# Performance work log

Hardware: AMD Instinct MI355X
Metric: run time of the kernel (lower is better)

## Reference

```python
import jax, jax.numpy as jnp
import numpy as np

D_MODEL = 512
DQ = D_MODEL // 4  # 128
TIME_SHIFT_START = 256
VELOCITY_START = 768
NOTE_OFF_START = 128


def conv1d(x, w, b, stride, pad):
    # x: [B, Cin, L], w: [Cout, Cin, K]
    y = jax.lax.conv_general_dilated(x, w, (stride,), [(pad, pad)],
                                     dimension_numbers=('NCH', 'OIH', 'NCH'))
    return y + b[None, :, None]


def adaptive_avg_pool1d(x, out_size):
    # faithful to torch AdaptiveAvgPool1d bin boundaries
    L = x.shape[-1]
    starts = (np.arange(out_size) * L) // out_size
    ends = np.ceil((np.arange(out_size) + 1) * L / out_size).astype(np.int64)
    cs = jnp.concatenate([jnp.zeros(x.shape[:-1] + (1,), x.dtype),
                          jnp.cumsum(x, axis=-1)], axis=-1)
    return (cs[..., ends] - cs[..., starts]) / jnp.asarray(ends - starts, x.dtype)


def setup_inputs() -> dict:
    key = jax.random.key(0)
    ks = jax.random.split(key, 20)

    def w(k, shape):
        fan_in = int(np.prod(shape[1:]))
        return jax.random.normal(k, shape, jnp.float32) / np.sqrt(fan_in)

    def b(k, n):
        return jax.random.normal(k, (n,), jnp.float32) * 0.01

    return {
        'tokens': jax.random.randint(ks[0], (32, 4096), 0, 774),
        'r1_w': w(ks[1], (32, 1, 8)),    'r1_b': b(ks[2], 32),
        'r2_w': w(ks[3], (64, 32, 4)),   'r2_b': b(ks[4], 64),
        'h1_w': w(ks[5], (64, 128, 12)), 'h1_b': b(ks[6], 64),
        'h2_w': w(ks[7], (32, 64, 8)),   'h2_b': b(ks[8], 32),
        'm1_w': w(ks[9], (64, 128, 5)),  'm1_b': b(ks[10], 64),
        'm2_w': w(ks[11], (32, 64, 3)),  'm2_b': b(ks[12], 32),
        'd1_w': w(ks[13], (16, 6, 4)),   'd1_b': b(ks[14], 16),
        'd2_w': w(ks[15], (16, 16, 3)),  'd2_b': b(ks[16], 16),
        'fc_w': w(ks[17], (D_MODEL, D_MODEL)), 'fc_b': b(ks[18], D_MODEL),
    }


def reference(tokens, r1_w, r1_b, r2_w, r2_b, h1_w, h1_b, h2_w, h2_b,
              m1_w, m1_b, m2_w, m2_b, d1_w, d1_b, d2_w, d2_b, fc_w, fc_b):
    B, S = tokens.shape
    relu = jax.nn.relu

    # rhythm: binary time-shift indicator [B,1,S]
    ts = ((tokens >= TIME_SHIFT_START) & (tokens < VELOCITY_START)).astype(jnp.float32)[:, None, :]
    r = relu(conv1d(ts, r1_w, r1_b, 2, 3))
    r = relu(conv1d(r, r2_w, r2_b, 2, 1))
    r = adaptive_avg_pool1d(r, DQ).reshape(B, -1)  # [B, 64*DQ]

    # vectorized one-hot pitch scatter (replaces the python double loop): [B,128,S]
    nm = tokens < NOTE_OFF_START
    pitch = jnp.transpose(
        jax.nn.one_hot(jnp.where(nm, tokens, 0) % 128, 128, dtype=jnp.float32)
        * nm[..., None].astype(jnp.float32), (0, 2, 1))

    h = relu(conv1d(pitch, h1_w, h1_b, 1, 6))
    h = relu(conv1d(h, h2_w, h2_b, 2, 3))
    h = adaptive_avg_pool1d(h, DQ).reshape(B, -1)  # [B, 32*DQ]

    m = relu(conv1d(pitch, m1_w, m1_b, 1, 2))
    m = relu(conv1d(m, m2_w, m2_b, 1, 1))
    m = adaptive_avg_pool1d(m, DQ).reshape(B, -1)  # [B, 32*DQ]

    # velocity one-hot scatter: [B,6,S]
    vm = tokens >= VELOCITY_START
    vel = jnp.clip(jnp.where(vm, tokens - VELOCITY_START, 0), 0, 5)
    vpat = jnp.transpose(
        jax.nn.one_hot(vel, 6, dtype=jnp.float32) * vm[..., None].astype(jnp.float32),
        (0, 2, 1))
    d = relu(conv1d(vpat, d1_w, d1_b, 1, 2))
    d = relu(conv1d(d, d2_w, d2_b, 1, 1))
    d = adaptive_avg_pool1d(d, DQ).reshape(B, -1)  # [B, 16*DQ]

    # total flattened size is 36*d_model != d_model, so torch branch always pools
    r, h, m, d = [adaptive_avg_pool1d(f[:, None, :], DQ)[:, 0] for f in (r, h, m, d)]

    combined = jnp.concatenate([r, h, m, d], axis=1)       # [B, d_model]
    feats = combined @ fc_w.T + fc_b                        # Linear
    return jnp.broadcast_to(feats[:, None, :], (B, S, D_MODEL))
```

## Files before the change

kernel.cpp:

```cpp
#include <hip/hip_runtime.h>

typedef unsigned short u16;
typedef unsigned int u32;
typedef float vf4 __attribute__((ext_vector_type(4)));
typedef unsigned int vu4 __attribute__((ext_vector_type(4)));
typedef short sh8 __attribute__((ext_vector_type(8)));
typedef float f32x4 __attribute__((ext_vector_type(4)));

__device__ __forceinline__ float bf2f(u16 u) {
  return __uint_as_float(((u32)u) << 16);
}
__device__ __forceinline__ u16 f2bf(float f) {
  u32 x = __float_as_uint(f);
  return (u16)((x + 0x7fffu + ((x >> 16) & 1u)) >> 16);
}
__device__ __forceinline__ float ldin(const void* p, int idx, int isf) {
  return isf ? ((const float*)p)[idx] : bf2f(((const u16*)p)[idx]);
}

#define OFF_FLAG  ((size_t)0)
#define OFF_WB    ((size_t)16)
#define OFF_WTH1  ((size_t)1180432)
#define OFF_WTM1  ((size_t)1576720)
#define OFF_COMB  ((size_t)1741840)
#define OFF_FEATF ((size_t)1807376)
#define OFF_FEATB ((size_t)1872912)
#define OFF_DP    ((size_t)18686736)
#define OFF_WH2B  ((size_t)52536080)
#define OFF_WH2L  ((size_t)52568848)
#define OFF_WM2B  ((size_t)52601616)
#define OFF_WM2L  ((size_t)52613904)
#define WS_NEEDED ((size_t)52626192)

#define WB_R1W 0
#define WB_R1B 256
#define WB_R2W 288
#define WB_R2B 8480
#define WB_H1B 8544
#define WB_H2W 8608
#define WB_H2B 24992
#define WB_M1B 25024
#define WB_M2W 25088
#define WB_M2B 31232
#define WB_D1W 31264
#define WB_D1B 31648
#define WB_D2W 31664
#define WB_D2B 32432
#define WB_FCW 32448
#define WB_FCB 294592
#define WB_TOTAL 295104

#define CV_TH1_END 394176
#define CV_TM1_END 435456
#define CV_CMB_END 451840
#define CV_WH2_END 468224
#define CV_TOTAL   474368

__global__ __launch_bounds__(256) void k_convert(
    const void* r1_w, const void* r1_b, const void* r2_w, const void* r2_b,
    const void* h1_w, const void* h1_b, const void* h2_w, const void* h2_b,
    const void* m1_w, const void* m1_b, const void* m2_w, const void* m2_b,
    const void* d1_w, const void* d1_b, const void* d2_w, const void* d2_b,
    const void* fc_w, const void* fc_b,
    int* __restrict__ flagp, float* __restrict__ wb,
    float* __restrict__ wTh1, float* __restrict__ wTm1,
    float* __restrict__ combined,
    u16* __restrict__ wh2b, u16* __restrict__ wh2l,
    u16* __restrict__ wm2b, u16* __restrict__ wm2l) {
  __shared__ int cnt[4];
  int tid = threadIdx.x;
  {
    u16 v = ((const u16*)fc_w)[2 * tid];
    int e = (v >> 7) & 0xFF;
    int outside = (e < 100 || e > 140) ? 1 : 0;
    unsigned long long m = __ballot(outside);
    if ((tid & 63) == 0) cnt[tid >> 6] = __popcll(m);
  }
  __syncthreads();
  int isf = (cnt[0] + cnt[1] + cnt[2] + cnt[3] >= 64) ? 1 : 0;
  if (blockIdx.x == 0 && tid == 0) flagp[0] = isf;

  int j = blockIdx.x * 256 + tid;
  if (j >= CV_TOTAL) return;
  if (j < WB_TOTAL) {
    const void* src; int si;
    if      (j < WB_R1B) { src = r1_w; si = j; }
    else if (j < WB_R2W) { src = r1_b; si = j - WB_R1B; }
    else if (j < WB_R2B) { src = r2_w; si = j - WB_R2W; }
    else if (j < WB_H1B) { src = r2_b; si = j - WB_R2B; }
    else if (j < WB_H2W) { src = h1_b; si = j - WB_H1B; }
    else if (j < WB_H2B) { src = h2_w; si = j - WB_H2W; }
    else if (j < WB_M1B) { src = h2_b; si = j - WB_H2B; }
    else if (j < WB_M2W) { src = m1_b; si = j - WB_M1B; }
    else if (j < WB_M2B) { src = m2_w; si = j - WB_M2W; }
    else if (j < WB_D1W) { src = m2_b; si = j - WB_M2B; }
    else if (j < WB_D1B) { src = d1_w; si = j - WB_D1W; }
    else if (j < WB_D2W) { src = d1_b; si = j - WB_D1B; }
    else if (j < WB_D2B) { src = d2_w; si = j - WB_D2W; }
    else if (j < WB_FCW) { src = d2_b; si = j - WB_D2B; }
    else if (j < WB_FCB) { src = fc_w; si = j - WB_FCW; }
    else                 { src = fc_b; si = j - WB_FCB; }
    wb[j] = ldin(src, si, isf);
  } else if (j < CV_TH1_END) {
    int j2 = j - WB_TOTAL;
    int o = j2 & 63, r = j2 >> 6;
    wTh1[j2] = (r >= 1536) ? 0.f : ldin(h1_w, (o * 128 + r / 12) * 12 + (r % 12), isf);
  } else if (j < CV_TM1_END) {
    int j3 = j - CV_TH1_END;
    int o = j3 & 63, r = j3 >> 6;
    wTm1[j3] = (r >= 640) ? 0.f : ldin(m1_w, (o * 128 + r / 5) * 5 + (r % 5), isf);
  } else if (j < CV_CMB_END) {
    combined[j - CV_TM1_END] = 0.f;
  } else if (j < CV_WH2_END) {
    int jj = j - CV_CMB_END;
    int o = jj >> 9, rem = jj & 511, c = rem >> 3, kk = rem & 7;
    float w = ldin(h2_w, (o * 64 + c) * 8 + kk, isf);
    u16 hi = f2bf(w);
    wh2b[jj] = hi;
    wh2l[jj] = f2bf(w - bf2f(hi));
  } else {
    int jj = j - CV_WH2_END;
    int o = jj / 192, rem = jj % 192, c = rem / 3, kk = rem % 3;
    float w = ldin(m2_w, (o * 64 + c) * 3 + kk, isf);
    u16 hi = f2bf(w);
    wm2b[jj] = hi;
    wm2l[jj] = f2bf(w - bf2f(hi));
  }
}


#define HT_STRIDE 142
#define MT_STRIDE 133

__device__ __forceinline__ void dev_hf(float* smem, const int* tok,
                                       const float* wTh1, const float* h1bf,
                                       const u16* wh2b, const u16* wh2l,
                                       const float* h2bf,
                                       float* combined, int chunk, int q, int b) {
  u16* htile = (u16*)smem;
  int* tks = (int*)(smem + 4544);
  const int tid = threadIdx.x;
  const int tb = q * 512 + chunk * 64;
  const int sg0 = 2 * tb;
  const int* tokb = tok + b * 4096;
  if (tid < 146) {
    int x = sg0 - 9 + tid;
    int p = ((unsigned)x < 4096u) ? tokb[x] : 128;
    tks[tid] = (p < 128 ? p : 128) * 768;
  }
  __syncthreads();
  {
    const int og = tid & 15, slot = tid >> 4;
    const float4 bias = *(const float4*)(h1bf + og * 4);
    const float* wbase = wTh1 + og * 4;
    for (int pos = slot; pos < 134; pos += 16) {
      int t = sg0 - 3 + pos;
      u16 o0 = 0, o1 = 0, o2 = 0, o3 = 0;
      if ((unsigned)t <= 4096u) {
        float4 acc = bias;
#pragma unroll
        for (int k = 0; k < 12; ++k) {
          const float4 wv = *(const float4*)(wbase + tks[pos + k] + k * 64);
          acc.x += wv.x; acc.y += wv.y; acc.z += wv.z; acc.w += wv.w;
        }
        o0 = f2bf(fmaxf(acc.x, 0.f)); o1 = f2bf(fmaxf(acc.y, 0.f));
        o2 = f2bf(fmaxf(acc.z, 0.f)); o3 = f2bf(fmaxf(acc.w, 0.f));
      }
      int rb = og * 4 * HT_STRIDE + pos;
      htile[rb] = o0;
      htile[rb + HT_STRIDE] = o1;
      htile[rb + 2 * HT_STRIDE] = o2;
      htile[rb + 3 * HT_STRIDE] = o3;
    }
  }
  __syncthreads();
  const int w = tid >> 6, l = tid & 63;
  const int quad = l >> 4, n = l & 15;
  const int ot = w & 1, tp = w >> 1;
  f32x4 acc2[2];
  acc2[0] = (f32x4){0.f, 0.f, 0.f, 0.f};
  acc2[1] = (f32x4){0.f, 0.f, 0.f, 0.f};
  const u16* wph = wh2b + (size_t)(16 * ot + n) * 512 + quad * 8;
  const u16* wpl = wh2l + (size_t)(16 * ot + n) * 512 + quad * 8;
  const u32* hp = (const u32*)htile;
  for (int kc = 0; kc < 2; ++kc) {
    sh8 ah[8], al[8];
#pragma unroll
    for (int s = 0; s < 8; ++s) {
      ah[s] = *(const sh8*)(wph + kc * 256 + 32 * s);
      al[s] = *(const sh8*)(wpl + kc * 256 + 32 * s);
    }
#pragma unroll
    for (int it = 0; it < 2; ++it) {
      int fb = 16 * (2 * it + tp) + n;
#pragma unroll
      for (int s = 0; s < 8; ++s) {
        int c = kc * 32 + 4 * s + quad;
        const u32* p = hp + c * 71 + fb;
        u32 bw[4] = {p[0], p[1], p[2], p[3]};
        sh8 bb;
        __builtin_memcpy(&bb, bw, 16);
        acc2[it] = __builtin_amdgcn_mfma_f32_16x16x32_bf16(ah[s], bb, acc2[it], 0, 0, 0);
        acc2[it] = __builtin_amdgcn_mfma_f32_16x16x32_bf16(al[s], bb, acc2[it], 0, 0, 0);
      }
    }
  }
#pragma unroll
  for (int r = 0; r < 4; ++r) {
    float bsv = h2bf[16 * ot + quad * 4 + r];
    float s = fmaxf(acc2[0][r] + bsv, 0.f) + fmaxf(acc2[1][r] + bsv, 0.f);
    s += __shfl_xor(s, 1, 64);
    s += __shfl_xor(s, 2, 64);
    s += __shfl_xor(s, 4, 64);
    s += __shfl_xor(s, 8, 64);
    if (n == 0) {
      int o = 16 * ot + quad * 4 + r;
      atomicAdd(&combined[b * 512 + 128 + 4 * o + q], s * (1.f / 512.f));
    }
  }
}

__device__ __forceinline__ void dev_mf(float* smem, const int* tok,
                                       const float* wTm1, const float* m1bf,
                                       const u16* wm2b, const u16* wm2l,
                                       const float* m2bf,
                                       float* combined, int sub, int q, int b) {
  u16* mtile = (u16*)smem;
  int* tks = (int*)(smem + 4256);
  const int tid = threadIdx.x;
  const int tb = q * 1024 + sub * 128;
  const int* tokb = tok + b * 4096;
  if (tid < 135) {
    int x = tb - 4 + tid;
    int p = ((unsigned)x < 4096u) ? tokb[x] : 128;
    tks[tid] = (p < 128 ? p : 128) * 320;
  }
  __syncthreads();
  {
    const int og = tid & 15, slot = tid >> 4;
    const float4 bias = *(const float4*)(m1bf + og * 4);
    const float* wbase = wTm1 + og * 4;
    for (int u = slot; u < 131; u += 16) {
      int t = tb - 2 + u;
      u16 o0 = 0, o1 = 0, o2 = 0, o3 = 0;
      if ((unsigned)t < 4096u) {
        float4 acc = bias;
#pragma unroll
        for (int k = 0; k < 5; ++k) {
          const float4 wv = *(const float4*)(wbase + tks[u + k] + k * 64);
          acc.x += wv.x; acc.y += wv.y; acc.z += wv.z; acc.w += wv.w;
        }
        o0 = f2bf(fmaxf(acc.x, 0.f)); o1 = f2bf(fmaxf(acc.y, 0.f));
        o2 = f2bf(fmaxf(acc.z, 0.f)); o3 = f2bf(fmaxf(acc.w, 0.f));
      }
      int rb = og * 4 * MT_STRIDE + u;
      mtile[rb] = o0;
      mtile[rb + MT_STRIDE] = o1;
      mtile[rb + 2 * MT_STRIDE] = o2;
      mtile[rb + 3 * MT_STRIDE] = o3;
    }
  }
  __syncthreads();
  const int w = tid >> 6, l = tid & 63;
  const int quad = l >> 4, n = l & 15;
  const int ot = w & 1, tp = w >> 1;
  sh8 ah[6], al[6];
  {
    const u16* wph = wm2b + (size_t)(16 * ot + n) * 192 + quad * 8;
    const u16* wpl = wm2l + (size_t)(16 * ot + n) * 192 + quad * 8;
#pragma unroll
    for (int s = 0; s < 6; ++s) {
      ah[s] = *(const sh8*)(wph + 32 * s);
      al[s] = *(const sh8*)(wpl + 32 * s);
    }
  }
  float bsv[4];
#pragma unroll
  for (int r = 0; r < 4; ++r) bsv[r] = m2bf[16 * ot + quad * 4 + r];
  float sm[4] = {0.f, 0.f, 0.f, 0.f};
  const int gkb = quad * 8;
  for (int it = 0; it < 4; ++it) {
    int ub = 16 * (2 * it + tp) + n + 1;
    f32x4 acc = {0.f, 0.f, 0.f, 0.f};
#pragma unroll
    for (int s = 0; s < 6; ++s) {
      sh8 bb;
#pragma unroll
      for (int j = 0; j < 8; ++j) {
        int gk = 32 * s + gkb + j;
        int c = (gk * 21846) >> 16;
        int kk = gk - 3 * c;
        bb[j] = (short)mtile[c * MT_STRIDE + ub + kk];
      }
      acc = __builtin_amdgcn_mfma_f32_16x16x32_bf16(ah[s], bb, acc, 0, 0, 0);
      acc = __builtin_amdgcn_mfma_f32_16x16x32_bf16(al[s], bb, acc, 0, 0, 0);
    }
#pragma unroll
    for (int r = 0; r < 4; ++r) sm[r] += fmaxf(acc[r] + bsv[r], 0.f);
  }
#pragma unroll
  for (int r = 0; r < 4; ++r) {
    float s = sm[r];
    s += __shfl_xor(s, 1, 64);
    s += __shfl_xor(s, 2, 64);
    s += __shfl_xor(s, 4, 64);
    s += __shfl_xor(s, 8, 64);
    if (n == 0) {
      int o = 16 * ot + quad * 4 + r;
      atomicAdd(&combined[b * 512 + 256 + 4 * o + q], s * (1.f / 1024.f));
    }
  }
}

__device__ __forceinline__ void dev_rf(float* smem, const int* tok,
                                       const float* r1wf, const float* r1bf,
                                       const float* r2wf, const float* r2bf,
                                       float* combined, int chunk, int b) {
  float* w1s = smem;
  float* b1s = smem + 256;
  float* Ibuf = smem + 288;
  float* r1t = smem + 560;
  float* wcr = smem + 4848;
  const int tid = threadIdx.x;
  const int tbase = chunk * 64;
  const int tk0 = 4 * tbase - 7;
  const int* tokb = tok + b * 4096;
  w1s[tid] = r1wf[tid];
  if (tid < 32) b1s[tid] = r1bf[tid];
  for (int i = tid; i < 270; i += 256) {
    int x = tk0 + i;
    float v = 0.f;
    if ((unsigned)x < 4096u) {
      int tk = tokb[x];
      v = (tk >= 256 && tk < 768) ? 1.f : 0.f;
    }
    Ibuf[i] = v;
  }
  __syncthreads();
  {
    const int tl1 = tid & 63, og1 = tid >> 6;
    for (int xi = tl1; xi < 134; xi += 64) {
      int x = 2 * tbase - 2 + xi;
      if ((unsigned)x < 2048u) {
        float iv[8];
#pragma unroll
        for (int k = 0; k < 8; ++k) iv[k] = Ibuf[2 * xi + k];
#pragma unroll
        for (int i = 0; i < 8; ++i) {
          int o = og1 * 8 + i;
          float a = b1s[o];
#pragma unroll
          for (int k = 0; k < 8; ++k) a = fmaf(w1s[o * 8 + k], iv[k], a);
          r1t[o * 134 + xi] = fmaxf(a, 0.f);
        }
      } else {
#pragma unroll
        for (int i = 0; i < 8; ++i) r1t[(og1 * 8 + i) * 134 + xi] = 0.f;
      }
    }
  }
  __syncthreads();
  const int half = chunk >> 3;
  const int og = tid >> 6, tl = tid & 63;
  float acc[16];
#pragma unroll
  for (int i = 0; i < 16; ++i) acc[i] = 0.f;
  for (int c0 = 0; c0 < 32; c0 += 8) {
    for (int f = tid; f < 2048; f += 256) {
      int o = f & 63, r = f >> 6, k = r & 3, cc = r >> 2;
      wcr[f] = r2wf[(o * 32 + c0 + cc) * 4 + k];
    }
    __syncthreads();
#pragma unroll
    for (int cc = 0; cc < 8; ++cc) {
      const float* rr = r1t + (c0 + cc) * 134 + 2 * tl;
      float ev[3], od[3];
#pragma unroll
      for (int f3 = 0; f3 < 3; ++f3) {
        ev[f3] = rr[2 * f3];
        od[f3] = rr[2 * f3 + 1];
      }
#pragma unroll
      for (int k = 0; k < 4; ++k) {
        const int p = (k + 1) & 1, fk = (k + 1) >> 1;
        const float* wv = &wcr[(cc * 4 + k) * 64 + og * 16];
        float4 wa = *(const float4*)wv;
        float4 wbv = *(const float4*)(wv + 4);
        float4 wcc = *(const float4*)(wv + 8);
        float4 wd4 = *(const float4*)(wv + 12);
        float wr[16] = {wa.x, wa.y, wa.z, wa.w, wbv.x, wbv.y, wbv.z, wbv.w,
                        wcc.x, wcc.y, wcc.z, wcc.w, wd4.x, wd4.y, wd4.z, wd4.w};
        float v0 = p ? od[fk] : ev[fk];
#pragma unroll
        for (int i = 0; i < 16; ++i) acc[i] = fmaf(v0, wr[i], acc[i]);
      }
    }
    __syncthreads();
  }
  const float inv = 1.f / 512.f;
#pragma unroll
  for (int i = 0; i < 16; ++i) {
    int o = og * 16 + i;
    float s = fmaxf(acc[i] + r2bf[o], 0.f);
#pragma unroll
    for (int d = 32; d > 0; d >>= 1) s += __shfl_down(s, d, 64);
    if (tl == 0) atomicAdd(&combined[b * 512 + 2 * o + half], s * inv);
  }
}

__device__ __forceinline__ void dev_df(float* smem, const int* tok,
                                       const float* d1wf, const float* d1bf,
                                       const float* d2wf, const float* d2bf,
                                       float* dpws, int chunk, int b) {
  float* wds7 = smem;
  float* wd = smem + 448;
  int* cls = (int*)(smem + 1216);
  float (*dt)[132] = reinterpret_cast<float(*)[132]>(smem + 1352);
  float* c2 = smem + 3464;
  const int tid = threadIdx.x;
  const int tbase = chunk * 128;
  const int* tokb = tok + b * 4096;
  for (int f = tid; f < 448; f += 256) {
    int k = f & 3, rest = f >> 2, v = rest % 7, c = rest / 7;
    wds7[f] = (v < 6) ? d1wf[(c * 6 + v) * 4 + k] : 0.f;
  }
  for (int f = tid; f < 768; f += 256) wd[f] = d2wf[f];
  if (tid < 136) {
    int x = tbase - 3 + tid;
    int v = 6;
    if ((unsigned)x < 4096u) {
      int tk = tokb[x];
      if (tk >= 768) { v = tk - 768; v = v > 5 ? 5 : v; } else v = 6;
    }
    cls[tid] = v;
  }
  __syncthreads();
  for (int f = tid; f < 16 * 131; f += 256) {
    int iu = f % 131, c = f / 131;
    int x = tbase - 1 + iu;
    float v = 0.f;
    if (x >= 0 && x <= 4096) {
      float a = d1bf[c];
#pragma unroll
      for (int k = 0; k < 4; ++k) {
        a += wds7[(c * 7 + cls[iu + k]) * 4 + k];
      }
      v = fmaxf(a, 0.f);
    }
    dt[c][iu] = v;
  }
  __syncthreads();
  for (int idx = tid; idx < 16 * 129; idx += 256) {
    int o = idx / 129, tl = idx % 129;
    float a = d2bf[o];
    const float* ww = &wd[o * 48];
#pragma unroll 4
    for (int c = 0; c < 16; ++c) {
      a = fmaf(dt[c][tl], ww[c * 3 + 0],
          fmaf(dt[c][tl + 1], ww[c * 3 + 1],
          fmaf(dt[c][tl + 2], ww[c * 3 + 2], a)));
    }
    c2[o * 133 + tl] = fmaxf(a, 0.f);
  }
  __syncthreads();
  if (tid < 64) {
    int o = tid >> 2, qq = tid & 3;
    const float* row = c2 + o * 133 + 32 * qq;
    float s = 0.f;
#pragma unroll
    for (int j = 0; j < 33; ++j) s += row[j];
    dpws[(size_t)(b * 16 + o) * 128 + 4 * chunk + qq] = s * (1.f / 33.f);
  }
}

__global__ __launch_bounds__(256, 4) void k_fused(const int* __restrict__ tok,
                                                  const float* __restrict__ wb,
                                                  const float* __restrict__ wTh1,
                                                  const float* __restrict__ wTm1,
                                                  const u16* __restrict__ wh2b,
                                                  const u16* __restrict__ wh2l,
                                                  const u16* __restrict__ wm2b,
                                                  const u16* __restrict__ wm2l,
                                                  float* __restrict__ combined,
                                                  float* __restrict__ dpws) {
  __shared__ __align__(16) float smem[6896];
  int bx = blockIdx.x;
  if (bx < 1024) {
    dev_hf(smem, tok, wTh1, wb + WB_H1B, wh2b, wh2l, wb + WB_H2B, combined,
           bx & 7, (bx >> 3) & 3, bx >> 5);
  } else if (bx < 2048) {
    int n = bx - 1024;
    dev_mf(smem, tok, wTm1, wb + WB_M1B, wm2b, wm2l, wb + WB_M2B, combined,
           n & 7, (n >> 3) & 3, n >> 5);
  } else if (bx < 2560) {
    int n = bx - 2048;
    dev_rf(smem, tok, wb + WB_R1W, wb + WB_R1B, wb + WB_R2W, wb + WB_R2B,
           combined, n & 15, n >> 4);
  } else {
    int n = bx - 2560;
    dev_df(smem, tok, wb + WB_D1W, wb + WB_D1B, wb + WB_D2W, wb + WB_D2B,
           dpws, n & 31, n >> 5);
  }
}

__global__ __launch_bounds__(256) void k_fc(const float* __restrict__ combined,
                                            const float* __restrict__ dpws,
                                            const float* __restrict__ fcwf,
                                            const float* __restrict__ fcbf,
                                            float* __restrict__ featf,
                                            u16* __restrict__ featb) {
  const int bx = blockIdx.x;
  const int b = bx >> 3, oct = bx & 7;
  const int tid = threadIdx.x;
  __shared__ float cb[512];
  cb[tid] = combined[b * 512 + tid];
  if (tid < 128) {
    cb[256 + tid] = combined[b * 512 + 256 + tid];
  } else {
    int j = tid - 128;
    int o = j >> 3, i0 = (j & 7) * 16;
    const float* row = dpws + (size_t)(b * 16 + o) * 128;
    float s = 0.f;
#pragma unroll
    for (int i = 0; i < 16; ++i) s += row[i0 + i];
    cb[384 + j] = s * (1.f / 16.f);
  }
  __syncthreads();
  const int oo = oct * 64 + (tid >> 2), part = tid & 3;
  float acc = 0.f;
  const float4* wr = (const float4*)(fcwf + (size_t)oo * 512 + part * 128);
#pragma unroll 8
  for (int j4 = 0; j4 < 32; ++j4) {
    float4 w = wr[j4];
    const float* c4 = &cb[part * 128 + j4 * 4];
    acc = fmaf(c4[0], w.x, acc);
    acc = fmaf(c4[1], w.y, acc);
    acc = fmaf(c4[2], w.z, acc);
    acc = fmaf(c4[3], w.w, acc);
  }
  acc += __shfl_xor(acc, 1, 64);
  acc += __shfl_xor(acc, 2, 64);
  if (part == 0) {
    float r = acc + fcbf[oo];
    featf[b * 512 + oo] = r;
    featb[b * 512 + oo] = f2bf(r);
  }
}

__global__ __launch_bounds__(256) void k_bcast(const int* __restrict__ flagp,
                                               const vf4* __restrict__ featf4,
                                               const vu4* __restrict__ featb4,
                                               vf4* __restrict__ outf,
                                               vu4* __restrict__ outb) {
  if (flagp[0]) {
    int base = blockIdx.x * 1024 + threadIdx.x;
#pragma unroll
    for (int s = 0; s < 4; ++s) {
      int g = base + s * 256;
      vf4 v = featf4[(g >> 19) * 128 + (g & 127)];
      __builtin_nontemporal_store(v, &outf[g]);
    }
  } else {
    int base = blockIdx.x * 512 + threadIdx.x;
#pragma unroll
    for (int s = 0; s < 2; ++s) {
      int g = base + s * 256;
      vu4 v = featb4[(g >> 18) * 64 + (g & 63)];
      __builtin_nontemporal_store(v, &outb[g]);
    }
  }
}

extern "C" void kernel_launch(void* const* d_in, const int* in_sizes, int n_in,
                              void* d_out, int out_size, void* d_ws, size_t ws_size,
                              hipStream_t stream) {
  if (ws_size < WS_NEEDED) return;

  const int* tokens = (const int*)d_in[0];
  const void* r1_w = d_in[1];  const void* r1_b = d_in[2];
  const void* r2_w = d_in[3];  const void* r2_b = d_in[4];
  const void* h1_w = d_in[5];  const void* h1_b = d_in[6];
  const void* h2_w = d_in[7];  const void* h2_b = d_in[8];
  const void* m1_w = d_in[9];  const void* m1_b = d_in[10];
  const void* m2_w = d_in[11]; const void* m2_b = d_in[12];
  const void* d1_w = d_in[13]; const void* d1_b = d_in[14];
  const void* d2_w = d_in[15]; const void* d2_b = d_in[16];
  const void* fc_w = d_in[17]; const void* fc_b = d_in[18];

  char* ws = (char*)d_ws;
  int*   flagp   = (int*)  (ws + OFF_FLAG);
  float* wb      = (float*)(ws + OFF_WB);
  float* wTh1    = (float*)(ws + OFF_WTH1);
  float* wTm1    = (float*)(ws + OFF_WTM1);
  float* combined= (float*)(ws + OFF_COMB);
  float* featf   = (float*)(ws + OFF_FEATF);
  u16*   featb   = (u16*)  (ws + OFF_FEATB);
  float* dpws    = (float*)(ws + OFF_DP);
  u16*   wh2b    = (u16*)  (ws + OFF_WH2B);
  u16*   wh2l    = (u16*)  (ws + OFF_WH2L);
  u16*   wm2b    = (u16*)  (ws + OFF_WM2B);
  u16*   wm2l    = (u16*)  (ws + OFF_WM2L);

  k_convert<<<1853, 256, 0, stream>>>(r1_w, r1_b, r2_w, r2_b, h1_w, h1_b, h2_w, h2_b,
                                      m1_w, m1_b, m2_w, m2_b, d1_w, d1_b, d2_w, d2_b,
                                      fc_w, fc_b, flagp, wb, wTh1, wTm1, combined,
                                      wh2b, wh2l, wm2b, wm2l);
  k_fused<<<3584, 256, 0, stream>>>(tokens, wb, wTh1, wTm1, wh2b, wh2l, wm2b, wm2l,
                                    combined, dpws);
  k_fc<<<256, 256, 0, stream>>>(combined, dpws, wb + WB_FCW, wb + WB_FCB, featf, featb);
  k_bcast<<<16384, 256, 0, stream>>>(flagp, (const vf4*)featf, (const vu4*)featb,
                                     (vf4*)d_out, (vu4*)d_out);
}
```

Baseline: 392.3 us.

## Fuse FC into broadcast kernel and interleave branch blocks in fused conv kernel

Merges the FC and broadcast kernels into one, so each of 2048 blocks recomputes a 64-output slice of the linear layer and writes it straight to 512 sequence rows. This drops one launch and the feature round trip through workspace. The FC work is now repeated 8 times per batch/octet, and the store pattern changes. Separately, the fused conv kernel's block index is interleaved modulo 7, so the heavy and light branches mix across the schedule and load balance better.

```diff
diff --git a/kernel.cpp b/kernel.cpp
--- a/kernel.cpp
+++ b/kernel.cpp
@@ -23,8 +23,6 @@
 #define OFF_WTH1  ((size_t)1180432)
 #define OFF_WTM1  ((size_t)1576720)
 #define OFF_COMB  ((size_t)1741840)
-#define OFF_FEATF ((size_t)1807376)
-#define OFF_FEATB ((size_t)1872912)
 #define OFF_DP    ((size_t)18686736)
 #define OFF_WH2B  ((size_t)52536080)
 #define OFF_WH2L  ((size_t)52568848)
@@ -485,34 +483,38 @@
                                                   float* __restrict__ dpws) {
   __shared__ __align__(16) float smem[6896];
   int bx = blockIdx.x;
-  if (bx < 1024) {
+  int s7 = bx % 7, i7 = bx / 7;
+  if (s7 < 2) {
+    int n = s7 * 512 + i7;
     dev_hf(smem, tok, wTh1, wb + WB_H1B, wh2b, wh2l, wb + WB_H2B, combined,
-           bx & 7, (bx >> 3) & 3, bx >> 5);
-  } else if (bx < 2048) {
-    int n = bx - 1024;
+           n & 7, (n >> 3) & 3, n >> 5);
+  } else if (s7 < 4) {
+    int n = (s7 - 2) * 512 + i7;
     dev_mf(smem, tok, wTm1, wb + WB_M1B, wm2b, wm2l, wb + WB_M2B, combined,
            n & 7, (n >> 3) & 3, n >> 5);
-  } else if (bx < 2560) {
-    int n = bx - 2048;
+  } else if (s7 < 5) {
+    int n = i7;
     dev_rf(smem, tok, wb + WB_R1W, wb + WB_R1B, wb + WB_R2W, wb + WB_R2B,
            combined, n & 15, n >> 4);
   } else {
-    int n = bx - 2560;
+    int n = (s7 - 5) * 512 + i7;
     dev_df(smem, tok, wb + WB_D1W, wb + WB_D1B, wb + WB_D2W, wb + WB_D2B,
            dpws, n & 31, n >> 5);
   }
 }
 
-__global__ __launch_bounds__(256) void k_fc(const float* __restrict__ combined,
-                                            const float* __restrict__ dpws,
-                                            const float* __restrict__ fcwf,
-                                            const float* __restrict__ fcbf,
-                                            float* __restrict__ featf,
-                                            u16* __restrict__ featb) {
+__global__ __launch_bounds__(256) void k_out(const int* __restrict__ flagp,
+                                             const float* __restrict__ combined,
+                                             const float* __restrict__ dpws,
+                                             const float* __restrict__ fcwf,
+                                             const float* __restrict__ fcbf,
+                                             float* __restrict__ outf,
+                                             u16* __restrict__ outb) {
   const int bx = blockIdx.x;
-  const int b = bx >> 3, oct = bx & 7;
+  const int s8 = bx & 7, oct = (bx >> 3) & 7, b = bx >> 6;
   const int tid = threadIdx.x;
   __shared__ float cb[512];
+  __shared__ float feat[64];
   cb[tid] = combined[b * 512 + tid];
   if (tid < 128) {
     cb[256 + tid] = combined[b * 512 + 256 + tid];
@@ -540,33 +542,29 @@
   }
   acc += __shfl_xor(acc, 1, 64);
   acc += __shfl_xor(acc, 2, 64);
-  if (part == 0) {
-    float r = acc + fcbf[oo];
-    featf[b * 512 + oo] = r;
-    featb[b * 512 + oo] = f2bf(r);
-  }
-}
-
-__global__ __launch_bounds__(256) void k_bcast(const int* __restrict__ flagp,
-                                               const vf4* __restrict__ featf4,
-                                               const vu4* __restrict__ featb4,
-                                               vf4* __restrict__ outf,
-                                               vu4* __restrict__ outb) {
+  if (part == 0) feat[tid >> 2] = acc + fcbf[oo];
+  __syncthreads();
+  const size_t obase = ((size_t)b * 4096 + (size_t)s8 * 512) * 512 + oct * 64;
   if (flagp[0]) {
-    int base = blockIdx.x * 1024 + threadIdx.x;
-#pragma unroll
-    for (int s = 0; s < 4; ++s) {
-      int g = base + s * 256;
-      vf4 v = featf4[(g >> 19) * 128 + (g & 127)];
-      __builtin_nontemporal_store(v, &outf[g]);
+    const int slot = tid & 15, rowg = tid >> 4;
+    float4 v4 = *(const float4*)&feat[slot * 4];
+    vf4 vv; vv[0] = v4.x; vv[1] = v4.y; vv[2] = v4.z; vv[3] = v4.w;
+    float* op = outf + obase + (size_t)rowg * 512 + slot * 4;
+#pragma unroll 8
+    for (int it = 0; it < 32; ++it) {
+      __builtin_nontemporal_store(vv, (vf4*)(op + (size_t)it * 16 * 512));
     }
   } else {
-    int base = blockIdx.x * 512 + threadIdx.x;
-#pragma unroll
-    for (int s = 0; s < 2; ++s) {
-      int g = base + s * 256;
-      vu4 v = featb4[(g >> 18) * 64 + (g & 63)];
-      __builtin_nontemporal_store(v, &outb[g]);
+    const int slot = tid & 7, rowg = tid >> 3;
+    u32 w0 = (u32)f2bf(feat[slot * 8 + 0]) | ((u32)f2bf(feat[slot * 8 + 1]) << 16);
+    u32 w1 = (u32)f2bf(feat[slot * 8 + 2]) | ((u32)f2bf(feat[slot * 8 + 3]) << 16);
+    u32 w2 = (u32)f2bf(feat[slot * 8 + 4]) | ((u32)f2bf(feat[slot * 8 + 5]) << 16);
+    u32 w3 = (u32)f2bf(feat[slot * 8 + 6]) | ((u32)f2bf(feat[slot * 8 + 7]) << 16);
+    vu4 vv; vv[0] = w0; vv[1] = w1; vv[2] = w2; vv[3] = w3;
+    u16* op = outb + obase + (size_t)rowg * 512 + slot * 8;
+#pragma unroll 8
+    for (int it = 0; it < 16; ++it) {
+      __builtin_nontemporal_store(vv, (vu4*)(op + (size_t)it * 32 * 512));
     }
   }
 }
@@ -593,8 +591,6 @@
   float* wTh1    = (float*)(ws + OFF_WTH1);
   float* wTm1    = (float*)(ws + OFF_WTM1);
   float* combined= (float*)(ws + OFF_COMB);
-  float* featf   = (float*)(ws + OFF_FEATF);
-  u16*   featb   = (u16*)  (ws + OFF_FEATB);
   float* dpws    = (float*)(ws + OFF_DP);
   u16*   wh2b    = (u16*)  (ws + OFF_WH2B);
   u16*   wh2l    = (u16*)  (ws + OFF_WH2L);
@@ -607,7 +603,6 @@
                                       wh2b, wh2l, wm2b, wm2l);
   k_fused<<<3584, 256, 0, stream>>>(tokens, wb, wTh1, wTm1, wh2b, wh2l, wm2b, wm2l,
                                     combined, dpws);
-  k_fc<<<256, 256, 0, stream>>>(combined, dpws, wb + WB_FCW, wb + WB_FCB, featf, featb);
-  k_bcast<<<16384, 256, 0, stream>>>(flagp, (const vf4*)featf, (const vu4*)featb,
-                                     (vf4*)d_out, (vu4*)d_out);
-}
+  k_out<<<2048, 256, 0, stream>>>(flagp, combined, dpws, wb + WB_FCW, wb + WB_FCB,
+                                  (float*)d_out, (u16*)d_out);
+}
```

After: 403.2 us. 1.03x slower.

## Transpose m-branch tile to time-major layout for vectorized MFMA operand loads

Applied to the files above, without the earlier changes.

Reorders the m2 weight layout to [kk][o][c] and stores the conv1 output tile time-major (time rows, 64 channels, padded stride 72). Each thread can then load an 8-element bf16 MFMA B operand with one vector LDS read instead of eight scalar gathered reads with division arithmetic. Conv1 outputs are written as a packed 64-bit store. This costs a slightly larger shared-memory footprint and changes the tks offset.

```diff
diff --git a/kernel.cpp b/kernel.cpp
--- a/kernel.cpp
+++ b/kernel.cpp
@@ -120,7 +120,7 @@
     wh2l[jj] = f2bf(w - bf2f(hi));
   } else {
     int jj = j - CV_WH2_END;
-    int o = jj / 192, rem = jj % 192, c = rem / 3, kk = rem % 3;
+    int kk = jj >> 11, rem = jj & 2047, o = rem >> 6, c = rem & 63;
     float w = ldin(m2_w, (o * 64 + c) * 3 + kk, isf);
     u16 hi = f2bf(w);
     wm2b[jj] = hi;
@@ -130,7 +130,7 @@
 
 
 #define HT_STRIDE 142
-#define MT_STRIDE 133
+#define MT2_STRIDE 72
 
 __device__ __forceinline__ void dev_hf(float* smem, const int* tok,
                                        const float* wTh1, const float* h1bf,
@@ -225,8 +225,8 @@
                                        const u16* wm2b, const u16* wm2l,
                                        const float* m2bf,
                                        float* combined, int sub, int q, int b) {
-  u16* mtile = (u16*)smem;
-  int* tks = (int*)(smem + 4256);
+  u16* mT = (u16*)smem;
+  int* tks = (int*)(smem + 4716);
   const int tid = threadIdx.x;
   const int tb = q * 1024 + sub * 128;
   const int* tokb = tok + b * 4096;
@@ -253,47 +253,45 @@
         o0 = f2bf(fmaxf(acc.x, 0.f)); o1 = f2bf(fmaxf(acc.y, 0.f));
         o2 = f2bf(fmaxf(acc.z, 0.f)); o3 = f2bf(fmaxf(acc.w, 0.f));
       }
-      int rb = og * 4 * MT_STRIDE + u;
-      mtile[rb] = o0;
-      mtile[rb + MT_STRIDE] = o1;
-      mtile[rb + 2 * MT_STRIDE] = o2;
-      mtile[rb + 3 * MT_STRIDE] = o3;
+      uint2 pack;
+      pack.x = (u32)o0 | ((u32)o1 << 16);
+      pack.y = (u32)o2 | ((u32)o3 << 16);
+      *(uint2*)&mT[u * MT2_STRIDE + og * 4] = pack;
     }
   }
   __syncthreads();
   const int w = tid >> 6, l = tid & 63;
   const int quad = l >> 4, n = l & 15;
   const int ot = w & 1, tp = w >> 1;
-  sh8 ah[6], al[6];
+  sh8 ah[3][2], al[3][2];
   {
-    const u16* wph = wm2b + (size_t)(16 * ot + n) * 192 + quad * 8;
-    const u16* wpl = wm2l + (size_t)(16 * ot + n) * 192 + quad * 8;
-#pragma unroll
-    for (int s = 0; s < 6; ++s) {
-      ah[s] = *(const sh8*)(wph + 32 * s);
-      al[s] = *(const sh8*)(wpl + 32 * s);
+    const u16* wph = wm2b + (size_t)(16 * ot + n) * 64 + quad * 8;
+    const u16* wpl = wm2l + (size_t)(16 * ot + n) * 64 + quad * 8;
+#pragma unroll
+    for (int kk = 0; kk < 3; ++kk) {
+#pragma unroll
+      for (int kc = 0; kc < 2; ++kc) {
+        ah[kk][kc] = *(const sh8*)(wph + kk * 2048 + kc * 32);
+        al[kk][kc] = *(const sh8*)(wpl + kk * 2048 + kc * 32);
+      }
     }
   }
   float bsv[4];
 #pragma unroll
   for (int r = 0; r < 4; ++r) bsv[r] = m2bf[16 * ot + quad * 4 + r];
   float sm[4] = {0.f, 0.f, 0.f, 0.f};
-  const int gkb = quad * 8;
   for (int it = 0; it < 4; ++it) {
-    int ub = 16 * (2 * it + tp) + n + 1;
+    const int un = 16 * (2 * it + tp) + n + 1;
     f32x4 acc = {0.f, 0.f, 0.f, 0.f};
 #pragma unroll
-    for (int s = 0; s < 6; ++s) {
-      sh8 bb;
-#pragma unroll
-      for (int j = 0; j < 8; ++j) {
-        int gk = 32 * s + gkb + j;
-        int c = (gk * 21846) >> 16;
-        int kk = gk - 3 * c;
-        bb[j] = (short)mtile[c * MT_STRIDE + ub + kk];
-      }
-      acc = __builtin_amdgcn_mfma_f32_16x16x32_bf16(ah[s], bb, acc, 0, 0, 0);
-      acc = __builtin_amdgcn_mfma_f32_16x16x32_bf16(al[s], bb, acc, 0, 0, 0);
+    for (int kk = 0; kk < 3; ++kk) {
+      const u16* rowp = mT + (un + kk) * MT2_STRIDE + quad * 8;
+#pragma unroll
+      for (int kc = 0; kc < 2; ++kc) {
+        sh8 bb = *(const sh8*)(rowp + kc * 32);
+        acc = __builtin_amdgcn_mfma_f32_16x16x32_bf16(ah[kk][kc], bb, acc, 0, 0, 0);
+        acc = __builtin_amdgcn_mfma_f32_16x16x32_bf16(al[kk][kc], bb, acc, 0, 0, 0);
+      }
     }
 #pragma unroll
     for (int r = 0; r < 4; ++r) sm[r] += fmaxf(acc[r] + bsv[r], 0.f);
```

Result: no change. 391.3 us (median of 2 runs) (-0.3%).
